# Kernel optimization log

Measured on AMD Instinct MI355X. Metric: run time of the kernel, lower is better.

The kernel has to match this reference:

```python
import jax, jax.numpy as jnp
import numpy as np

SPARSITY_W = 0.01
SMOOTH_W = 0.1
K = 10  # min(10, N-1) with N >> 10


def setup_inputs() -> dict:
    key = jax.random.key(0)
    k1, k2, k3 = jax.random.split(key, 3)
    N = 16384
    positions = jax.random.normal(k1, (N, 3), dtype=jnp.float32)
    opacities = jax.random.uniform(k2, (N,), dtype=jnp.float32)
    scales = jax.random.uniform(k3, (N, 3), dtype=jnp.float32)
    return {"positions": positions, "opacities": opacities, "scales": scales}


def _pairwise_dist(x):
    # Euclidean cdist(x, x): [N, N]
    sq = jnp.sum(x * x, axis=-1)
    d2 = sq[:, None] + sq[None, :] - 2.0 * (x @ x.T)
    return jnp.sqrt(jnp.maximum(d2, 0.0))


def reference(positions, opacities, scales):
    # sparsity: mean |opacity|
    sparsity_loss = jnp.mean(jnp.abs(opacities))

    # smoothness: kNN (k=10, excluding self) gather + mean |opacity diff|
    dist = _pairwise_dist(positions)                       # [N, N]
    _, idx = jax.lax.top_k(-dist, K + 1)                   # smallest K+1 dists
    nbr_idx = idx[:, 1:]                                   # drop self: [N, K]
    nbr_op = opacities[nbr_idx]                            # [N, K]
    smoothness_loss = jnp.mean(jnp.abs(opacities[:, None] - nbr_op))

    # scale reg: mean |scale - 1|
    scale_loss = jnp.mean(jnp.abs(scales - 1.0))

    # opacity reg: mean (opacity - 0.5)^2
    opacity_loss = jnp.mean((opacities - 0.5) ** 2)

    return (SPARSITY_W * sparsity_loss + SMOOTH_W * smoothness_loss
            + scale_loss + opacity_loss)
```

## Files before the change

### kernel.cpp

```cpp
#include <hip/hip_runtime.h>
#include <stdint.h>

#define NPTS   16384
#define TOPK   10
#define NBX    32
#define NBK    (32 * 32 * 32)
#define XMIN   (-5.0f)
#define INVBW  (3.2f)
#define SENT_STEP 0x4000u
#define LIGHT_MAX 512u
#define HEAVY_GRID 1024
#define NSLOT  64


__device__ __forceinline__ unsigned umin_(unsigned a, unsigned b) { return a < b ? a : b; }
__device__ __forceinline__ unsigned umax_(unsigned a, unsigned b) { return a > b ? a : b; }

__device__ __forceinline__ void chain_insert(unsigned a[TOPK], unsigned key) {
#pragma unroll
    for (int k = TOPK - 1; k > 0; --k) a[k] = umin_(umax_(a[k - 1], key), a[k]);
    a[0] = umin_(a[0], key);
}

__device__ __forceinline__ void ce_(unsigned &x, unsigned &y) {
    unsigned lo = umin_(x, y); y = umax_(x, y); x = lo;
}

__device__ __forceinline__ void bitonic10(unsigned a[TOPK]) {
    ce_(a[0], a[8]); ce_(a[1], a[9]);
    ce_(a[0], a[4]); ce_(a[1], a[5]); ce_(a[2], a[6]); ce_(a[3], a[7]);
    ce_(a[0], a[2]); ce_(a[1], a[3]); ce_(a[4], a[6]); ce_(a[5], a[7]);
    ce_(a[0], a[1]); ce_(a[2], a[3]); ce_(a[4], a[5]); ce_(a[6], a[7]); ce_(a[8], a[9]);
}

__device__ __forceinline__ void merge_shfl(unsigned a[TOPK], int w) {
    unsigned b[TOPK];
#pragma unroll
    for (int k = 0; k < TOPK; ++k) b[k] = (unsigned)__shfl_xor((int)a[k], w, 64);
#pragma unroll
    for (int k = 0; k < TOPK; ++k) a[k] = umin_(a[k], b[TOPK - 1 - k]);
    bitonic10(a);
}

__device__ __forceinline__ void scan2(
    unsigned a[TOPK], const float4* __restrict__ sorted,
    unsigned p0, unsigned p1, unsigned s, float mx, float my, float mz)
{
    float4 c0 = sorted[p0];
    float4 c1 = sorted[p1];
    float dx0 = c0.x - mx, dy0 = c0.y - my, dz0 = c0.z - mz;
    float dx1 = c1.x - mx, dy1 = c1.y - my, dz1 = c1.z - mz;
    float d20 = fmaf(dx0, dx0, fmaf(dy0, dy0, dz0 * dz0));
    float d21 = fmaf(dx1, dx1, fmaf(dy1, dy1, dz1 * dz1));
    unsigned k0 = (__float_as_uint(d20) & 0xFFFFC000u) | p0;
    unsigned k1 = (__float_as_uint(d21) & 0xFFFFC000u) | p1;
    if (p0 == s) k0 = 0xFFFFFFFFu;
    if (p1 == s) k1 = 0xFFFFFFFFu;
    unsigned kmin = umin_(k0, k1), kmax = umax_(k0, k1);
    if (kmin < a[TOPK - 1]) {
        chain_insert(a, kmin);
        if (kmax < a[TOPK - 1]) chain_insert(a, kmax);
    }
}

__device__ __forceinline__ void scan1(
    unsigned a[TOPK], const float4* __restrict__ sorted,
    unsigned p, unsigned s, float mx, float my, float mz)
{
    float4 c = sorted[p];
    float dx = c.x - mx, dy = c.y - my, dz = c.z - mz;
    float d2 = fmaf(dx, dx, fmaf(dy, dy, dz * dz));
    unsigned key = (__float_as_uint(d2) & 0xFFFFC000u) | p;
    if (p == s) key = 0xFFFFFFFFu;
    if (key < a[TOPK - 1]) chain_insert(a, key);
}

__device__ __forceinline__ int cellf(float v) {
    int b = (int)((v - XMIN) * INVBW);
    return min(max(b, 0), NBX - 1);
}

__global__ __launch_bounds__(256) void setup_kernel(
    const float* __restrict__ pos, const float* __restrict__ opac,
    const float* __restrict__ scales, float* __restrict__ parts,
    unsigned* __restrict__ hist)
{
    int i = blockIdx.x * 256 + threadIdx.x;
    float o = opac[i];
    float d = o - 0.5f;
    float s_sp = fabsf(o);
    float s_op = d * d;
    float s_sc = fabsf(scales[3 * i] - 1.0f) + fabsf(scales[3 * i + 1] - 1.0f)
               + fabsf(scales[3 * i + 2] - 1.0f);
    int bx = cellf(pos[3 * i]);
    int by = cellf(pos[3 * i + 1]);
    int bz = cellf(pos[3 * i + 2]);
    atomicAdd(&hist[(bx << 10) | (by << 5) | bz], 1u);
#pragma unroll
    for (int off = 32; off > 0; off >>= 1) {
        s_sp += __shfl_down(s_sp, off, 64);
        s_sc += __shfl_down(s_sc, off, 64);
        s_op += __shfl_down(s_op, off, 64);
    }
    if ((threadIdx.x & 63) == 0) {
        const int row = (blockIdx.x * 4 + (threadIdx.x >> 6)) & (NSLOT - 1);
        atomicAdd(&parts[row * 32 + 0], s_sp);
        atomicAdd(&parts[row * 32 + 1], s_sc);
        atomicAdd(&parts[row * 32 + 2], s_op);
    }
}

__global__ __launch_bounds__(1024) void prefix_scan(
    unsigned* __restrict__ hist, unsigned* __restrict__ base)
{
    __shared__ unsigned wsum[16];
    const int t = threadIdx.x;
    const int lane = t & 63, wid = t >> 6;
    unsigned loc[32];
    uint4* h4 = (uint4*)(hist + t * 32);
#pragma unroll
    for (int j = 0; j < 8; ++j) {
        uint4 h = h4[j];
        loc[4 * j + 0] = h.x; loc[4 * j + 1] = h.y;
        loc[4 * j + 2] = h.z; loc[4 * j + 3] = h.w;
    }
    unsigned run = 0;
#pragma unroll
    for (int j = 0; j < 32; ++j) { unsigned v = loc[j]; loc[j] = run; run += v; }
    unsigned inc = run;
#pragma unroll
    for (int off = 1; off < 64; off <<= 1) {
        unsigned v = (unsigned)__shfl_up((int)inc, off, 64);
        if (lane >= off) inc += v;
    }
    if (lane == 63) wsum[wid] = inc;
    __syncthreads();
    if (wid == 0) {
        unsigned w = (lane < 16) ? wsum[lane] : 0u;
#pragma unroll
        for (int off = 1; off < 16; off <<= 1) {
            unsigned v = (unsigned)__shfl_up((int)w, off, 64);
            if (lane >= off) w += v;
        }
        if (lane < 16) wsum[lane] = w;
    }
    __syncthreads();
    const unsigned wbase = (wid > 0) ? wsum[wid - 1] : 0u;
    const unsigned tbase = wbase + inc - run;
    uint4* b4 = (uint4*)(base + t * 32);
#pragma unroll
    for (int j = 0; j < 8; ++j) {
        b4[j] = make_uint4(loc[4 * j] + tbase, loc[4 * j + 1] + tbase,
                           loc[4 * j + 2] + tbase, loc[4 * j + 3] + tbase);
        h4[j] = make_uint4(0u, 0u, 0u, 0u);
    }
    if (t == 1023) base[NBK] = NPTS;
}

__global__ __launch_bounds__(256) void scatter_sorted(
    const float* __restrict__ pos, const float* __restrict__ opac,
    const unsigned* __restrict__ base, unsigned* __restrict__ cnt,
    float4* __restrict__ sorted)
{
    int i = blockIdx.x * 256 + threadIdx.x;
    float x = pos[3 * i], y = pos[3 * i + 1], z = pos[3 * i + 2];
    int b = (cellf(x) << 10) | (cellf(y) << 5) | cellf(z);
    unsigned p = base[b] + atomicAdd(&cnt[b], 1u);
    sorted[p] = make_float4(x, y, z, opac[i]);
}

__global__ __launch_bounds__(256) void knn_main(
    const float4* __restrict__ sorted, const unsigned* __restrict__ base,
    unsigned* __restrict__ r2m, float* __restrict__ parts)
{
    const int sub = threadIdx.x & 15;
    const int wid = threadIdx.x >> 6;
    const int s   = blockIdx.x * 16 + (threadIdx.x >> 4);

    const float4 me = sorted[s];

    unsigned a[TOPK];
#pragma unroll
    for (int k = 0; k < TOPK; ++k) a[k] = 0xFFFFFFFFu;
    {
        const int dir = sub >> 3;
        const int start = 1 + (sub & 7) * 16;
#pragma unroll 4
        for (int t = 0; t < 16; ++t) {
            int p = dir ? (s - start - t) : (s + start + t);
            int pc = min(max(p, 0), NPTS - 1);
            float4 c = sorted[pc];
            float dx = c.x - me.x, dy = c.y - me.y, dz = c.z - me.z;
            float d2 = fmaf(dx, dx, fmaf(dy, dy, dz * dz));
            unsigned key = (__float_as_uint(d2) & 0xFFFFC000u) | (unsigned)pc;
            if (p < 0 || p >= NPTS) key = 0xFFFFFFFFu;
            chain_insert(a, key);
        }
    }
    merge_shfl(a, 1); merge_shfl(a, 2); merge_shfl(a, 4); merge_shfl(a, 8);
    const unsigned sentinel = (a[TOPK - 1] & 0xFFFFC000u) + SENT_STEP;
    const float R = sqrtf(__uint_as_float(sentinel)) + 1e-6f;

    const int bxlo = cellf(me.x - R), bxhi = cellf(me.x + R);
    const int bylo = cellf(me.y - R), byhi = cellf(me.y + R);
    const int bzlo = cellf(me.z - R), bzhi = cellf(me.z + R);
    const int nyw   = byhi - bylo + 1;
    const int npair = (bxhi - bxlo + 1) * nyw;

    const int q0  = sub / nyw, r0  = sub - q0 * nyw;
    const int q16 = 16 / nyw,  r16 = 16 - q16 * nyw;

    unsigned csum = 0;
    {
        int bx = bxlo + q0, byo = r0;
        for (int pi = sub; pi < npair; pi += 16) {
            int cb = (bx << 10) | ((bylo + byo) << 5);
            csum += base[cb + bzhi + 1] - base[cb + bzlo];
            byo += r16; bx += q16;
            if (byo >= nyw) { byo -= nyw; ++bx; }
        }
    }
#pragma unroll
    for (int off = 1; off <= 8; off <<= 1)
        csum += (unsigned)__shfl_xor((int)csum, off, 64);
    const bool heavy = csum > LIGHT_MAX;
    if (sub == 0) r2m[s] = heavy ? sentinel : 0u;

#pragma unroll
    for (int k = 0; k < TOPK; ++k) a[k] = sentinel;
    if (!heavy) {
        int bx = bxlo + q0, byo = r0;
        int pi = sub;
        unsigned lo = 0, hi = 0;
        if (pi < npair) {
            int cb = (bx << 10) | ((bylo + byo) << 5);
            lo = base[cb + bzlo]; hi = base[cb + bzhi + 1];
        }
        while (pi < npair) {
            const int npi = pi + 16;
            byo += r16; bx += q16;
            if (byo >= nyw) { byo -= nyw; ++bx; }
            unsigned nlo = 0, nhi = 0;
            if (npi < npair) {
                int cb = (bx << 10) | ((bylo + byo) << 5);
                nlo = base[cb + bzlo]; nhi = base[cb + bzhi + 1];
            }
            unsigned p = lo;
            for (; p + 1 < hi; p += 2)
                scan2(a, sorted, p, p + 1, (unsigned)s, me.x, me.y, me.z);
            if (p < hi)
                scan1(a, sorted, p, (unsigned)s, me.x, me.y, me.z);
            pi = npi; lo = nlo; hi = nhi;
        }
        merge_shfl(a, 1); merge_shfl(a, 2); merge_shfl(a, 4); merge_shfl(a, 8);
    }

    float v = 0.0f;
    if (!heavy && sub < TOPK) {
        int j = (int)(a[sub] & 0x3FFFu);
        v = fabsf(me.w - sorted[j].w);
    }
    v += __shfl_down(v, 8, 64);
    v += __shfl_down(v, 4, 64);
    v += __shfl_down(v, 2, 64);
    v += __shfl_down(v, 1, 64);
    float g = (sub == 0) ? v : 0.0f;
    g += __shfl_down(g, 16, 64);
    g += __shfl_down(g, 32, 64);
    if ((threadIdx.x & 63) == 0) {
        const int row = (blockIdx.x * 4 + wid) & (NSLOT - 1);
        atomicAdd(&parts[row * 32 + 3], g);
    }
}

__global__ __launch_bounds__(256) void knn_heavy(
    const float4* __restrict__ sorted, const unsigned* __restrict__ r2m,
    const unsigned* __restrict__ base, float* __restrict__ parts)
{
    const int lane = threadIdx.x & 63;
    const int wave = (blockIdx.x * 256 + threadIdx.x) >> 6;
    const int nw   = HEAVY_GRID * 4;

    float wsum = 0.0f;
    for (int s = wave; s < NPTS; s += nw) {
        const unsigned sentinel = r2m[s];
        if (sentinel == 0u) continue;
        const float4 me = sorted[s];
        const float R = sqrtf(__uint_as_float(sentinel)) + 1e-6f;

        const int bxlo = cellf(me.x - R), bxhi = cellf(me.x + R);
        const int bylo = cellf(me.y - R), byhi = cellf(me.y + R);
        const int bzlo = cellf(me.z - R), bzhi = cellf(me.z + R);
        const int nyw   = byhi - bylo + 1;
        const int npair = (bxhi - bxlo + 1) * nyw;

        unsigned a[TOPK];
#pragma unroll
        for (int k = 0; k < TOPK; ++k) a[k] = sentinel;

        for (int pi = lane; pi < npair; pi += 64) {
            int cbx = bxlo + pi / nyw, cby = bylo + pi % nyw;
            int cb = (cbx << 10) | (cby << 5);
            unsigned lo = base[cb + bzlo], hi = base[cb + bzhi + 1];
            unsigned p = lo;
            for (; p + 1 < hi; p += 2)
                scan2(a, sorted, p, p + 1, (unsigned)s, me.x, me.y, me.z);
            if (p < hi)
                scan1(a, sorted, p, (unsigned)s, me.x, me.y, me.z);
        }

        merge_shfl(a, 1);  merge_shfl(a, 2);  merge_shfl(a, 4);
        merge_shfl(a, 8);  merge_shfl(a, 16); merge_shfl(a, 32);

        float v = 0.0f;
        if (lane < TOPK) {
            int j = (int)(a[lane] & 0x3FFFu);
            v = fabsf(me.w - sorted[j].w);
        }
        v += __shfl_down(v, 8, 64);
        v += __shfl_down(v, 4, 64);
        v += __shfl_down(v, 2, 64);
        v += __shfl_down(v, 1, 64);
        wsum += v;
    }
    if (lane == 0 && wsum != 0.0f)
        atomicAdd(&parts[(wave & (NSLOT - 1)) * 32 + 3], wsum);
}

__global__ void combine(const float* __restrict__ parts, float* __restrict__ out)
{
    const int lane = threadIdx.x;
    float4 p = *(const float4*)(parts + lane * 32);
    float sp = p.x, sc = p.y, op = p.z, sm = p.w;
#pragma unroll
    for (int off = 32; off > 0; off >>= 1) {
        sp += __shfl_down(sp, off, 64);
        sc += __shfl_down(sc, off, 64);
        op += __shfl_down(op, off, 64);
        sm += __shfl_down(sm, off, 64);
    }
    if (lane == 0) {
        const float n = (float)NPTS;
        out[0] = 0.01f * (sp / n) + 0.1f * (sm / (n * 10.0f))
               + sc / (3.0f * n) + op / n;
    }
}

extern "C" void kernel_launch(void* const* d_in, const int* in_sizes, int n_in,
                              void* d_out, int out_size, void* d_ws, size_t ws_size,
                              hipStream_t stream)
{
    const float* pos    = (const float*)d_in[0];
    const float* opac   = (const float*)d_in[1];
    const float* scales = (const float*)d_in[2];
    float* out = (float*)d_out;

    char* ws = (char*)d_ws;
    float*    parts  = (float*)(ws + 128);
    unsigned* histcnt= (unsigned*)(ws + 8448);
    unsigned* base   = (unsigned*)(ws + 139520);
    unsigned* r2m    = (unsigned*)(ws + 270720);
    float4*   sorted = (float4*)(ws + 336256);

    hipMemsetAsync(ws, 0, 139520, stream);

    setup_kernel  <<<NPTS / 256, 256, 0, stream>>>(pos, opac, scales, parts, histcnt);
    prefix_scan   <<<1, 1024, 0, stream>>>(histcnt, base);
    scatter_sorted<<<NPTS / 256, 256, 0, stream>>>(pos, opac, base, histcnt, sorted);
    knn_main      <<<NPTS / 16, 256, 0, stream>>>(sorted, base, r2m, parts);
    knn_heavy     <<<HEAVY_GRID, 256, 0, stream>>>(sorted, r2m, base, parts);
    combine       <<<1, 64, 0, stream>>>(parts, out);
}
```

Before: 136.6 us.

## Merge light and heavy kNN kernels into one wave-per-query kernel

Drops the light/heavy split and gives each query point a full 64-lane wave. The lanes fetch cell ranges cooperatively, broadcast them with shuffles, and scan each cell's points strided across lanes. This removes the extra kernel launch, the per-query cell-count pre-pass and the r2m buffer, and it balances work inside dense cells. The cost is four times as many waves, with many lanes idle when cells are sparse. The accumulation slots are also widened to 256 to reduce contention on the atomics.

```diff
diff --git a/kernel.cpp b/kernel.cpp
--- a/kernel.cpp
+++ b/kernel.cpp
@@ -8,9 +8,7 @@
 #define XMIN   (-5.0f)
 #define INVBW  (3.2f)
 #define SENT_STEP 0x4000u
-#define LIGHT_MAX 512u
-#define HEAVY_GRID 1024
-#define NSLOT  64
+#define NSLOT  256
 
 
 __device__ __forceinline__ unsigned umin_(unsigned a, unsigned b) { return a < b ? a : b; }
@@ -40,27 +38,6 @@
 #pragma unroll
     for (int k = 0; k < TOPK; ++k) a[k] = umin_(a[k], b[TOPK - 1 - k]);
     bitonic10(a);
-}
-
-__device__ __forceinline__ void scan2(
-    unsigned a[TOPK], const float4* __restrict__ sorted,
-    unsigned p0, unsigned p1, unsigned s, float mx, float my, float mz)
-{
-    float4 c0 = sorted[p0];
-    float4 c1 = sorted[p1];
-    float dx0 = c0.x - mx, dy0 = c0.y - my, dz0 = c0.z - mz;
-    float dx1 = c1.x - mx, dy1 = c1.y - my, dz1 = c1.z - mz;
-    float d20 = fmaf(dx0, dx0, fmaf(dy0, dy0, dz0 * dz0));
-    float d21 = fmaf(dx1, dx1, fmaf(dy1, dy1, dz1 * dz1));
-    unsigned k0 = (__float_as_uint(d20) & 0xFFFFC000u) | p0;
-    unsigned k1 = (__float_as_uint(d21) & 0xFFFFC000u) | p1;
-    if (p0 == s) k0 = 0xFFFFFFFFu;
-    if (p1 == s) k1 = 0xFFFFFFFFu;
-    unsigned kmin = umin_(k0, k1), kmax = umax_(k0, k1);
-    if (kmin < a[TOPK - 1]) {
-        chain_insert(a, kmin);
-        if (kmax < a[TOPK - 1]) chain_insert(a, kmax);
-    }
 }
 
 __device__ __forceinline__ void scan1(
@@ -169,13 +146,12 @@
     sorted[p] = make_float4(x, y, z, opac[i]);
 }
 
-__global__ __launch_bounds__(256) void knn_main(
+__global__ __launch_bounds__(256) void knn_all(
     const float4* __restrict__ sorted, const unsigned* __restrict__ base,
-    unsigned* __restrict__ r2m, float* __restrict__ parts)
-{
-    const int sub = threadIdx.x & 15;
-    const int wid = threadIdx.x >> 6;
-    const int s   = blockIdx.x * 16 + (threadIdx.x >> 4);
+    float* __restrict__ parts)
+{
+    const int lane = threadIdx.x & 63;
+    const int s    = (blockIdx.x * 256 + threadIdx.x) >> 6;
 
     const float4 me = sorted[s];
 
@@ -183,10 +159,10 @@
 #pragma unroll
     for (int k = 0; k < TOPK; ++k) a[k] = 0xFFFFFFFFu;
     {
-        const int dir = sub >> 3;
-        const int start = 1 + (sub & 7) * 16;
-#pragma unroll 4
-        for (int t = 0; t < 16; ++t) {
+        const int dir = lane >> 5;
+        const int start = 1 + (lane & 31) * 4;
+#pragma unroll
+        for (int t = 0; t < 4; ++t) {
             int p = dir ? (s - start - t) : (s + start + t);
             int pc = min(max(p, 0), NPTS - 1);
             float4 c = sorted[pc];
@@ -197,7 +173,8 @@
             chain_insert(a, key);
         }
     }
-    merge_shfl(a, 1); merge_shfl(a, 2); merge_shfl(a, 4); merge_shfl(a, 8);
+    merge_shfl(a, 1);  merge_shfl(a, 2);  merge_shfl(a, 4);
+    merge_shfl(a, 8);  merge_shfl(a, 16); merge_shfl(a, 32);
     const unsigned sentinel = (a[TOPK - 1] & 0xFFFFC000u) + SENT_STEP;
     const float R = sqrtf(__uint_as_float(sentinel)) + 1e-6f;
 
@@ -207,131 +184,52 @@
     const int nyw   = byhi - bylo + 1;
     const int npair = (bxhi - bxlo + 1) * nyw;
 
-    const int q0  = sub / nyw, r0  = sub - q0 * nyw;
-    const int q16 = 16 / nyw,  r16 = 16 - q16 * nyw;
-
-    unsigned csum = 0;
-    {
-        int bx = bxlo + q0, byo = r0;
-        for (int pi = sub; pi < npair; pi += 16) {
-            int cb = (bx << 10) | ((bylo + byo) << 5);
-            csum += base[cb + bzhi + 1] - base[cb + bzlo];
-            byo += r16; bx += q16;
-            if (byo >= nyw) { byo -= nyw; ++bx; }
-        }
-    }
-#pragma unroll
-    for (int off = 1; off <= 8; off <<= 1)
-        csum += (unsigned)__shfl_xor((int)csum, off, 64);
-    const bool heavy = csum > LIGHT_MAX;
-    if (sub == 0) r2m[s] = heavy ? sentinel : 0u;
-
 #pragma unroll
     for (int k = 0; k < TOPK; ++k) a[k] = sentinel;
-    if (!heavy) {
-        int bx = bxlo + q0, byo = r0;
-        int pi = sub;
-        unsigned lo = 0, hi = 0;
+
+    for (int cbase = 0; cbase < npair; cbase += 64) {
+        const int cnum = min(64, npair - cbase);
+        unsigned mylo = 0, myhi = 0;
+        const int pi = cbase + lane;
         if (pi < npair) {
-            int cb = (bx << 10) | ((bylo + byo) << 5);
-            lo = base[cb + bzlo]; hi = base[cb + bzhi + 1];
-        }
-        while (pi < npair) {
-            const int npi = pi + 16;
-            byo += r16; bx += q16;
-            if (byo >= nyw) { byo -= nyw; ++bx; }
-            unsigned nlo = 0, nhi = 0;
-            if (npi < npair) {
-                int cb = (bx << 10) | ((bylo + byo) << 5);
-                nlo = base[cb + bzlo]; nhi = base[cb + bzhi + 1];
-            }
-            unsigned p = lo;
-            for (; p + 1 < hi; p += 2)
-                scan2(a, sorted, p, p + 1, (unsigned)s, me.x, me.y, me.z);
-            if (p < hi)
+            const int qx = pi / nyw;
+            const int cb = ((bxlo + qx) << 10) | ((bylo + pi - qx * nyw) << 5);
+            mylo = base[cb + bzlo];
+            myhi = base[cb + bzhi + 1];
+        }
+        for (int j = 0; j < cnum; ++j) {
+            const unsigned lo = (unsigned)__shfl((int)mylo, j, 64);
+            const unsigned hi = (unsigned)__shfl((int)myhi, j, 64);
+            for (unsigned p = lo + lane; p < hi; p += 64)
                 scan1(a, sorted, p, (unsigned)s, me.x, me.y, me.z);
-            pi = npi; lo = nlo; hi = nhi;
-        }
-        merge_shfl(a, 1); merge_shfl(a, 2); merge_shfl(a, 4); merge_shfl(a, 8);
-    }
+        }
+    }
+
+    merge_shfl(a, 1);  merge_shfl(a, 2);  merge_shfl(a, 4);
+    merge_shfl(a, 8);  merge_shfl(a, 16); merge_shfl(a, 32);
 
     float v = 0.0f;
-    if (!heavy && sub < TOPK) {
-        int j = (int)(a[sub] & 0x3FFFu);
+    if (lane < TOPK) {
+        int j = (int)(a[lane] & 0x3FFFu);
         v = fabsf(me.w - sorted[j].w);
     }
     v += __shfl_down(v, 8, 64);
     v += __shfl_down(v, 4, 64);
     v += __shfl_down(v, 2, 64);
     v += __shfl_down(v, 1, 64);
-    float g = (sub == 0) ? v : 0.0f;
-    g += __shfl_down(g, 16, 64);
-    g += __shfl_down(g, 32, 64);
-    if ((threadIdx.x & 63) == 0) {
-        const int row = (blockIdx.x * 4 + wid) & (NSLOT - 1);
-        atomicAdd(&parts[row * 32 + 3], g);
-    }
-}
-
-__global__ __launch_bounds__(256) void knn_heavy(
-    const float4* __restrict__ sorted, const unsigned* __restrict__ r2m,
-    const unsigned* __restrict__ base, float* __restrict__ parts)
-{
-    const int lane = threadIdx.x & 63;
-    const int wave = (blockIdx.x * 256 + threadIdx.x) >> 6;
-    const int nw   = HEAVY_GRID * 4;
-
-    float wsum = 0.0f;
-    for (int s = wave; s < NPTS; s += nw) {
-        const unsigned sentinel = r2m[s];
-        if (sentinel == 0u) continue;
-        const float4 me = sorted[s];
-        const float R = sqrtf(__uint_as_float(sentinel)) + 1e-6f;
-
-        const int bxlo = cellf(me.x - R), bxhi = cellf(me.x + R);
-        const int bylo = cellf(me.y - R), byhi = cellf(me.y + R);
-        const int bzlo = cellf(me.z - R), bzhi = cellf(me.z + R);
-        const int nyw   = byhi - bylo + 1;
-        const int npair = (bxhi - bxlo + 1) * nyw;
-
-        unsigned a[TOPK];
-#pragma unroll
-        for (int k = 0; k < TOPK; ++k) a[k] = sentinel;
-
-        for (int pi = lane; pi < npair; pi += 64) {
-            int cbx = bxlo + pi / nyw, cby = bylo + pi % nyw;
-            int cb = (cbx << 10) | (cby << 5);
-            unsigned lo = base[cb + bzlo], hi = base[cb + bzhi + 1];
-            unsigned p = lo;
-            for (; p + 1 < hi; p += 2)
-                scan2(a, sorted, p, p + 1, (unsigned)s, me.x, me.y, me.z);
-            if (p < hi)
-                scan1(a, sorted, p, (unsigned)s, me.x, me.y, me.z);
-        }
-
-        merge_shfl(a, 1);  merge_shfl(a, 2);  merge_shfl(a, 4);
-        merge_shfl(a, 8);  merge_shfl(a, 16); merge_shfl(a, 32);
-
-        float v = 0.0f;
-        if (lane < TOPK) {
-            int j = (int)(a[lane] & 0x3FFFu);
-            v = fabsf(me.w - sorted[j].w);
-        }
-        v += __shfl_down(v, 8, 64);
-        v += __shfl_down(v, 4, 64);
-        v += __shfl_down(v, 2, 64);
-        v += __shfl_down(v, 1, 64);
-        wsum += v;
-    }
-    if (lane == 0 && wsum != 0.0f)
-        atomicAdd(&parts[(wave & (NSLOT - 1)) * 32 + 3], wsum);
+    if (lane == 0)
+        atomicAdd(&parts[(s & (NSLOT - 1)) * 32 + 3], v);
 }
 
 __global__ void combine(const float* __restrict__ parts, float* __restrict__ out)
 {
     const int lane = threadIdx.x;
-    float4 p = *(const float4*)(parts + lane * 32);
-    float sp = p.x, sc = p.y, op = p.z, sm = p.w;
+    float sp = 0.0f, sc = 0.0f, op = 0.0f, sm = 0.0f;
+#pragma unroll
+    for (int r = 0; r < NSLOT / 64; ++r) {
+        float4 p = *(const float4*)(parts + (r * 64 + lane) * 32);
+        sp += p.x; sc += p.y; op += p.z; sm += p.w;
+    }
 #pragma unroll
     for (int off = 32; off > 0; off >>= 1) {
         sp += __shfl_down(sp, off, 64);
@@ -357,17 +255,15 @@
 
     char* ws = (char*)d_ws;
     float*    parts  = (float*)(ws + 128);
-    unsigned* histcnt= (unsigned*)(ws + 8448);
-    unsigned* base   = (unsigned*)(ws + 139520);
-    unsigned* r2m    = (unsigned*)(ws + 270720);
-    float4*   sorted = (float4*)(ws + 336256);
-
-    hipMemsetAsync(ws, 0, 139520, stream);
+    unsigned* histcnt= (unsigned*)(ws + 33024);
+    unsigned* base   = (unsigned*)(ws + 164096);
+    float4*   sorted = (float4*)(ws + 295296);
+
+    hipMemsetAsync(ws, 0, 164096, stream);
 
     setup_kernel  <<<NPTS / 256, 256, 0, stream>>>(pos, opac, scales, parts, histcnt);
     prefix_scan   <<<1, 1024, 0, stream>>>(histcnt, base);
     scatter_sorted<<<NPTS / 256, 256, 0, stream>>>(pos, opac, base, histcnt, sorted);
-    knn_main      <<<NPTS / 16, 256, 0, stream>>>(sorted, base, r2m, parts);
-    knn_heavy     <<<HEAVY_GRID, 256, 0, stream>>>(sorted, r2m, base, parts);
+    knn_all       <<<NPTS / 4, 256, 0, stream>>>(sorted, base, parts);
     combine       <<<1, 64, 0, stream>>>(parts, out);
 }
```

Result: faster. 133.6 us (-2.2%).
